# Optimization experiments

Hardware: AMD Instinct MI355X
Metric: run time of the kernel (lower is better)

Reference implementation:

```python
import jax, jax.numpy as jnp
import numpy as np

B, S1, S2, H = 8, 2048, 2048, 1024

def setup_inputs() -> dict:
    key = jax.random.key(0)
    k1, k2, kw, kb = jax.random.split(key, 4)
    hidden1 = jax.random.normal(k1, (B, S1, H), dtype=jnp.float32)
    hidden2 = jax.random.normal(k2, (B, S2, H), dtype=jnp.float32)
    W = jax.random.normal(kw, (H, H), dtype=jnp.float32) * 0.001
    bias = jax.random.normal(kb, (1,), dtype=jnp.float32) * 0.02
    return {"hidden1": hidden1, "hidden2": hidden2, "W": W, "bias": bias}

def reference(hidden1, hidden2, W, bias):
    # weight[b, i, j] = (hidden1 @ W)[b, i, :] . hidden2[b, j, :] + bias
    weight = jnp.einsum('bih,hk,bjk->bij', hidden1, W, hidden2) + bias[0]  # (B, S1, S2)
    # softmax over s1 (dim=1), then transpose-bmm with hidden1 -> (B, S2, H)
    a1 = jax.nn.softmax(weight, axis=1)
    hidden_1 = jnp.einsum('bij,bih->bjh', a1, hidden1)
    # softmax over s2 (dim=2), bmm with hidden2 -> (B, S1, H)
    a2 = jax.nn.softmax(weight, axis=2)
    hidden_2 = jnp.einsum('bij,bjh->bih', a2, hidden2)
    return (hidden_1, hidden_2)
```

## Files before the change

### kernel.cpp

```cpp
#include <hip/hip_runtime.h>
#include <stdint.h>

#define B_  8
#define S1_ 2048
#define S2_ 2048
#define H_  1024

typedef __attribute__((ext_vector_type(8))) short bf16x8;
typedef __attribute__((ext_vector_type(4))) float f32x4;
typedef unsigned short u16;

__device__ __forceinline__ u16 f2bf(float f){
  union { float f; uint32_t v; } x; x.f = f;
  uint32_t r = x.v + 0x7fffu + ((x.v >> 16) & 1u);
  return (u16)(r >> 16);
}
__device__ __forceinline__ u16 f2h(float f){
  union { _Float16 h; u16 u; } c; c.h = (_Float16)f; return c.u;
}
__device__ __forceinline__ float h2f(u16 u){
  union { _Float16 h; u16 u; } c; c.u = u; return (float)c.h;
}
__device__ __forceinline__ uint32_t pk2bf(float lo, float hi){
  uint32_t r;
  asm("v_cvt_pk_bf16_f32 %0, %1, %2" : "=v"(r) : "v"(lo), "v"(hi));
  return r;
}
__device__ __forceinline__ void async16(void* lds, const void* g){
  __builtin_amdgcn_global_load_lds(
      (const __attribute__((address_space(1))) uint32_t*)g,
      (__attribute__((address_space(3))) uint32_t*)lds, 16, 0, 0);
}

__global__ __launch_bounds__(256) void k_cvt_bf16(const float* __restrict__ in,
                                                  u16* __restrict__ out, long n){
  long i = ((long)blockIdx.x * 256 + threadIdx.x) * 8;
  const long stride = (long)gridDim.x * 256 * 8;
  for (; i < n; i += stride){
    float4 a = *(const float4*)(in + i);
    float4 b = *(const float4*)(in + i + 4);
    union { bf16x8 v; uint32_t w[4]; } o;
    o.w[0] = pk2bf(a.x, a.y); o.w[1] = pk2bf(a.z, a.w);
    o.w[2] = pk2bf(b.x, b.y); o.w[3] = pk2bf(b.z, b.w);
    *(bf16x8*)(out + i) = o.v;
  }
}

__global__ __launch_bounds__(256) void k_tcvt(const float* __restrict__ in,
                                              u16* __restrict__ out, int R, int Cc){
  __shared__ u16 t[32][33];
  in  += (long)blockIdx.z * R * Cc;
  out += (long)blockIdx.z * R * Cc;
  const int x = threadIdx.x & 31, y0 = threadIdx.x >> 5;
  const int bx = blockIdx.x * 32, by = blockIdx.y * 32;
  for (int r = y0; r < 32; r += 8) t[r][x] = f2bf(in[(long)(by + r) * Cc + bx + x]);
  __syncthreads();
  for (int r = y0; r < 32; r += 8) out[(long)(bx + r) * R + by + x] = t[x][r];
}

__global__ __launch_bounds__(256) void k_cvtT2(const float* __restrict__ in,
                                               u16* __restrict__ out_n,
                                               u16* __restrict__ out_t, int R, int Cc){
  __shared__ u16 t[64][68];
  in    += (long)blockIdx.z * R * Cc;
  out_n += (long)blockIdx.z * R * Cc;
  out_t += (long)blockIdx.z * R * Cc;
  const int tid = threadIdx.x;
  const int r0 = tid >> 4;
  const int c4 = (tid & 15) * 4;
  const int bx = blockIdx.x * 64;
  const int by = blockIdx.y * 64;
#pragma unroll
  for (int it = 0; it < 4; ++it){
    const int r = it*16 + r0;
    float4 v = *(const float4*)(in + (long)(by + r)*Cc + bx + c4);
    u16 b0 = f2bf(v.x), b1 = f2bf(v.y), b2 = f2bf(v.z), b3 = f2bf(v.w);
    ushort4 o; o.x = b0; o.y = b1; o.z = b2; o.w = b3;
    *(ushort4*)(out_n + (long)(by + r)*Cc + bx + c4) = o;
    t[r][c4] = b0; t[r][c4+1] = b1; t[r][c4+2] = b2; t[r][c4+3] = b3;
  }
  __syncthreads();
#pragma unroll
  for (int it = 0; it < 4; ++it){
    const int c = it*16 + r0;
    ushort4 o;
    o.x = t[c4  ][c]; o.y = t[c4+1][c]; o.z = t[c4+2][c]; o.w = t[c4+3][c];
    *(ushort4*)(out_t + (long)(bx + c)*R + by + c4) = o;
  }
}

template<int OM, bool STATS>
__global__ __launch_bounds__(512) void k_gemm256(
    const u16* __restrict__ A, const u16* __restrict__ Bm, void* __restrict__ Cv,
    int M, int N, int K, long sA, long sB, long sC,
    float* __restrict__ rpmax, float* __restrict__ rpsum,
    float* __restrict__ cpmax, float* __restrict__ cpsum)
{
  const int GX = gridDim.x, GY = gridDim.y;
  const long plane = (long)GX * GY;
  const long tot = plane * gridDim.z;
  const long lin = blockIdx.x + (long)GX * (blockIdx.y + (long)GY * blockIdx.z);
  const long chunk = tot >> 3;
  const long swz = (lin & 7) * chunk + (lin >> 3);
  const int bz = (int)(swz / plane);
  const int rr = (int)(swz % plane);
  const int by_ = rr / GX, bx_ = rr % GX;

  A += (long)bz * sA; Bm += (long)bz * sB;
  __shared__ u16 lds[4 * 16384];
  const int tid = threadIdx.x, lane = tid & 63, w = tid >> 6;
  const int wm = w >> 2, wn = w & 3;
  const int brow = bx_ * 256, bcol = by_ * 256;

  f32x4 acc[8][4];
#pragma unroll
  for (int m=0;m<8;++m)
#pragma unroll
    for (int n=0;n<4;++n) acc[m][n] = (f32x4){0.f,0.f,0.f,0.f};

  const int fr = lane & 15;
  const int g8s = ((lane >> 4) ^ ((lane >> 1) & 3)) * 8;

  const int cc0 = w*128 + lane;
  const int cc1 = w*128 + 64 + lane;
  const int sl0 = (cc0 & 3) ^ ((cc0 >> 3) & 3);
  const int sl1 = (cc1 & 3) ^ ((cc1 >> 3) & 3);
  const u16* gA0 = A  + (long)(brow + (cc0 >> 2)) * K + sl0*8;
  const u16* gA1 = A  + (long)(brow + (cc1 >> 2)) * K + sl1*8;
  const u16* gB0 = Bm + (long)(bcol + (cc0 >> 2)) * K + sl0*8;
  const u16* gB1 = Bm + (long)(bcol + (cc1 >> 2)) * K + sl1*8;
  const int ldA0 = (w*128)*8, ldA1 = (w*128 + 64)*8;

  auto stage = [&](int buf, int t){
    u16* base = lds + buf*16384;
    async16(base + ldA0,        gA0 + t*32);
    async16(base + ldA1,        gA1 + t*32);
    async16(base + 8192 + ldA0, gB0 + t*32);
    async16(base + 8192 + ldA1, gB1 + t*32);
  };
  auto ldfrag = [&](int buf, bf16x8* a, bf16x8* b){
    const u16* At = lds + buf*16384;
    const u16* Bt = At + 8192;
#pragma unroll
    for (int n=0;n<4;++n) b[n] = *(const bf16x8*)(Bt + (wn*64 + n*16 + fr)*32 + g8s);
#pragma unroll
    for (int m=0;m<8;++m) a[m] = *(const bf16x8*)(At + (wm*128 + m*16 + fr)*32 + g8s);
  };

  const int NT = K >> 5;
  stage(0,0); stage(1,1); stage(2,2);
  asm volatile("s_waitcnt vmcnt(4)" ::: "memory");
  __builtin_amdgcn_s_barrier();

  bf16x8 a0[8], b0[4], a1[8], b1[4];
  ldfrag(0, a0, b0);

  for (int t = 0; t < NT; t += 2){
    if (t + 3 < NT) stage((t+3)&3, t+3);
    ldfrag((t+1)&3, a1, b1);
    __builtin_amdgcn_sched_barrier(0);
    __builtin_amdgcn_s_setprio(1);
#pragma unroll
    for (int m=0;m<8;++m)
#pragma unroll
      for (int n=0;n<4;++n)
        acc[m][n] = __builtin_amdgcn_mfma_f32_16x16x32_bf16(a0[m], b0[n], acc[m][n], 0,0,0);
    __builtin_amdgcn_s_setprio(0);
    asm volatile("s_waitcnt vmcnt(4)" ::: "memory");
    __builtin_amdgcn_s_barrier();

    if (t + 4 < NT) stage((t+4)&3, t+4);
    if (t + 2 < NT) ldfrag((t+2)&3, a0, b0);
    __builtin_amdgcn_sched_barrier(0);
    __builtin_amdgcn_s_setprio(1);
#pragma unroll
    for (int m=0;m<8;++m)
#pragma unroll
      for (int n=0;n<4;++n)
        acc[m][n] = __builtin_amdgcn_mfma_f32_16x16x32_bf16(a1[m], b1[n], acc[m][n], 0,0,0);
    __builtin_amdgcn_s_setprio(0);
    if (t + 2 < NT){
      asm volatile("s_waitcnt vmcnt(4)" ::: "memory");
      __builtin_amdgcn_s_barrier();
    }
  }

  const int crow = brow + wm*128 + (lane >> 4) * 4;
  const int ccol = bcol + wn*64 + fr;
  if constexpr (OM == 2){
    float* C = (float*)Cv + (long)bz * sC;
#pragma unroll
    for (int m=0;m<8;++m)
#pragma unroll
      for (int n=0;n<4;++n){
        f32x4 v = acc[m][n];
        float* cp = C + (long)(crow + m*16) * N + ccol + n*16;
#pragma unroll
        for (int q=0;q<4;++q) cp[(long)q*N] = v[q];
      }
  } else {
    u16* C = (u16*)Cv + (long)bz * sC;
#pragma unroll
    for (int m=0;m<8;++m)
#pragma unroll
      for (int n=0;n<4;++n){
        f32x4 v = acc[m][n];
        u16* cp = C + (long)(crow + m*16) * N + ccol + n*16;
#pragma unroll
        for (int q=0;q<4;++q) cp[(long)q*N] = OM ? f2h(v[q]) : f2bf(v[q]);
      }
  }

  if constexpr (STATS){
    const int hi = lane >> 4;
#pragma unroll
    for (int m=0;m<8;++m){
      f32x4 mx = acc[m][0];
#pragma unroll
      for (int n=1;n<4;++n)
#pragma unroll
        for (int q=0;q<4;++q) mx[q] = fmaxf(mx[q], acc[m][n][q]);
#pragma unroll
      for (int off=1; off<16; off<<=1)
#pragma unroll
        for (int q=0;q<4;++q) mx[q] = fmaxf(mx[q], __shfl_xor(mx[q], off));
      f32x4 sm = (f32x4){0.f,0.f,0.f,0.f};
#pragma unroll
      for (int n=0;n<4;++n)
#pragma unroll
        for (int q=0;q<4;++q) sm[q] += __expf(acc[m][n][q] - mx[q]);
#pragma unroll
      for (int off=1; off<16; off<<=1)
#pragma unroll
        for (int q=0;q<4;++q) sm[q] += __shfl_xor(sm[q], off);
      if (fr == 0){
        const int nb = by_*4 + wn;
        const long rb = ((long)bz*32 + nb)*2048 + brow + wm*128 + m*16 + hi*4;
#pragma unroll
        for (int q=0;q<4;++q){ rpmax[rb+q] = mx[q]; rpsum[rb+q] = sm[q]; }
      }
    }
#pragma unroll
    for (int n=0;n<4;++n){
      float mx = acc[0][n][0];
#pragma unroll
      for (int m=0;m<8;++m)
#pragma unroll
        for (int q=0;q<4;++q) mx = fmaxf(mx, acc[m][n][q]);
      mx = fmaxf(mx, __shfl_xor(mx, 16));
      mx = fmaxf(mx, __shfl_xor(mx, 32));
      float sm = 0.f;
#pragma unroll
      for (int m=0;m<8;++m)
#pragma unroll
        for (int q=0;q<4;++q) sm += __expf(acc[m][n][q] - mx);
      sm += __shfl_xor(sm, 16);
      sm += __shfl_xor(sm, 32);
      if (hi == 0){
        const int mb = bx_*2 + wm;
        const long cb = ((long)bz*16 + mb)*2048 + bcol + wn*64 + n*16 + fr;
        cpmax[cb] = mx; cpsum[cb] = sm;
      }
    }
  }
}

__global__ __launch_bounds__(256) void k_combine(
    const float* __restrict__ rpmax, const float* __restrict__ rpsum,
    const float* __restrict__ cpmax, const float* __restrict__ cpsum,
    float* __restrict__ rmax, float* __restrict__ rinv,
    float* __restrict__ cmax, float* __restrict__ cinv)
{
  const long i = (long)blockIdx.x*256 + threadIdx.x;
  const int b = (int)(i >> 11), r = (int)(i & 2047);
  if (blockIdx.y == 0){
    const float* pm = rpmax + ((long)b*32)*2048 + r;
    const float* ps = rpsum + ((long)b*32)*2048 + r;
    float m = -3.4e38f;
#pragma unroll
    for (int k=0;k<32;++k) m = fmaxf(m, pm[(long)k*2048]);
    float s = 0.f;
#pragma unroll
    for (int k=0;k<32;++k) s += ps[(long)k*2048] * __expf(pm[(long)k*2048] - m);
    rmax[i] = m; rinv[i] = 1.f / s;
  } else {
    const float* pm = cpmax + ((long)b*16)*2048 + r;
    const float* ps = cpsum + ((long)b*16)*2048 + r;
    float m = -3.4e38f;
#pragma unroll
    for (int k=0;k<16;++k) m = fmaxf(m, pm[(long)k*2048]);
    float s = 0.f;
#pragma unroll
    for (int k=0;k<16;++k) s += ps[(long)k*2048] * __expf(pm[(long)k*2048] - m);
    cmax[i] = m; cinv[i] = 1.f / s;
  }
}

__global__ __launch_bounds__(256) void k_p1t(u16* __restrict__ Wg, u16* __restrict__ P2,
                                             const float* __restrict__ cmax,
                                             const float* __restrict__ cinv,
                                             const float* __restrict__ rmax,
                                             const float* __restrict__ rinv){
  const int ti = blockIdx.x, tj = blockIdx.y;
  if (tj < ti) return;
  const int b = blockIdx.z;
  u16* S = Wg + (long)b * S1_ * S2_;
  const int jl = threadIdx.x & 63, ig = threadIdx.x >> 6;
  const int I0 = ti*64, J0 = tj*64;
  const float cmA = cmax[b*S2_ + J0 + jl], ciA = cinv[b*S2_ + J0 + jl];
  const float cmB = cmax[b*S2_ + I0 + jl], ciB = cinv[b*S2_ + I0 + jl];
  float ra[16], rc[16];
#pragma unroll
  for (int q=0;q<16;++q) ra[q] = h2f(S[(long)(I0 + ig*16 + q)*S2_ + J0 + jl]);
#pragma unroll
  for (int q=0;q<16;++q) rc[q] = h2f(S[(long)(J0 + ig*16 + q)*S2_ + I0 + jl]);

  if (P2){
    u16* P2b = P2 + (long)b * S1_ * S2_;
#pragma unroll
    for (int q=0;q<16;++q){
      const int r = I0 + ig*16 + q;
      P2b[(long)r*S2_ + J0 + jl] = f2bf(__expf(ra[q] - rmax[b*S1_+r]) * rinv[b*S1_+r]);
    }
    if (ti != tj){
#pragma unroll
      for (int q=0;q<16;++q){
        const int r = J0 + ig*16 + q;
        P2b[(long)r*S2_ + I0 + jl] = f2bf(__expf(rc[q] - rmax[b*S1_+r]) * rinv[b*S1_+r]);
      }
    }
  }

  float a[16], c[16];
#pragma unroll
  for (int q=0;q<16;++q) a[q] = __expf(ra[q] - cmA) * ciA;
#pragma unroll
  for (int q=0;q<16;++q) c[q] = __expf(rc[q] - cmB) * ciB;
  __syncthreads();
  union { bf16x8 v; uint32_t w4[4]; } o0, o1;
#pragma unroll
  for (int k=0;k<4;++k){ o0.w4[k] = pk2bf(a[2*k], a[2*k+1]); o1.w4[k] = pk2bf(a[8+2*k], a[9+2*k]); }
  *(bf16x8*)(S + (long)(J0+jl)*S2_ + I0 + ig*16)     = o0.v;
  *(bf16x8*)(S + (long)(J0+jl)*S2_ + I0 + ig*16 + 8) = o1.v;
#pragma unroll
  for (int k=0;k<4;++k){ o0.w4[k] = pk2bf(c[2*k], c[2*k+1]); o1.w4[k] = pk2bf(c[8+2*k], c[9+2*k]); }
  *(bf16x8*)(S + (long)(I0+jl)*S2_ + J0 + ig*16)     = o0.v;
  *(bf16x8*)(S + (long)(I0+jl)*S2_ + J0 + ig*16 + 8) = o1.v;
}

__global__ __launch_bounds__(256) void k_gemm_h2(
    const u16* __restrict__ Wg, const u16* __restrict__ Bt, float* __restrict__ C,
    const float* __restrict__ rmax, const float* __restrict__ rinv)
{
  const int b = blockIdx.z;
  const u16* A  = Wg + (long)b * S1_ * S2_;
  const u16* Bp = Bt + (long)b * H_ * S2_;
  float* Cp = C + (long)b * S1_ * H_;

  __shared__ u16 As[128*32];
  __shared__ u16 Bs[128*32];
  const int tid = threadIdx.x, lane = tid & 63, w = tid >> 6;
  const int wr = (w >> 1) * 64, wc = (w & 1) * 64;
  const int brow = blockIdx.x * 128, bcol = blockIdx.y * 128;
  f32x4 acc[4][4];
#pragma unroll
  for (int m=0;m<4;++m)
#pragma unroll
    for (int n=0;n<4;++n) acc[m][n] = (f32x4){0.f,0.f,0.f,0.f};

  const int arow = w*16 + (lane >> 2);
  const int scol = (lane & 3) * 8;
  const u16* gA0 = A + (long)(brow + arow) * S2_ + scol;
  const u16* gA1 = gA0 + (long)64 * S2_;
  const float rm0 = rmax[b*S1_ + brow + arow],      ri0 = rinv[b*S1_ + brow + arow];
  const float rm1 = rmax[b*S1_ + brow + arow + 64], ri1 = rinv[b*S1_ + brow + arow + 64];
  u16* wA0 = As + arow*32 + scol;
  u16* wA1 = As + (arow+64)*32 + scol;

  const u16* gb = Bp + (long)(bcol + arow) * S2_ + scol;
  u16* lB0 = Bs + (w*16)*32;  u16* lB1 = Bs + (64 + w*16)*32;

  const int koff = (lane >> 4) * 8;
  const int fr = lane & 15;

  for (int k0 = 0; k0 < S2_; k0 += 32){
    bf16x8 x0 = *(const bf16x8*)(gA0 + k0);
    bf16x8 x1 = *(const bf16x8*)(gA1 + k0);
    async16(lB0, gb);  async16(lB1, gb + (long)64*S2_);
    gb += 32;
    union { bf16x8 v; uint32_t w4[4]; } y0, y1;
#pragma unroll
    for (int k=0;k<4;++k){
      y0.w4[k] = pk2bf(__expf(h2f((u16)x0[2*k])   - rm0) * ri0,
                       __expf(h2f((u16)x0[2*k+1]) - rm0) * ri0);
      y1.w4[k] = pk2bf(__expf(h2f((u16)x1[2*k])   - rm1) * ri1,
                       __expf(h2f((u16)x1[2*k+1]) - rm1) * ri1);
    }
    *(bf16x8*)wA0 = y0.v;
    *(bf16x8*)wA1 = y1.v;
    __syncthreads();
    bf16x8 af[4], bf[4];
#pragma unroll
    for (int m=0;m<4;++m) af[m] = *(const bf16x8*)(As + (wr + m*16 + fr)*32 + koff);
#pragma unroll
    for (int n=0;n<4;++n) bf[n] = *(const bf16x8*)(Bs + (wc + n*16 + fr)*32 + koff);
#pragma unroll
    for (int m=0;m<4;++m)
#pragma unroll
      for (int n=0;n<4;++n)
        acc[m][n] = __builtin_amdgcn_mfma_f32_16x16x32_bf16(af[m], bf[n], acc[m][n], 0,0,0);
    __syncthreads();
  }
  const int crow = brow + wr + (lane >> 4) * 4;
  const int ccol = bcol + wc + fr;
#pragma unroll
  for (int m=0;m<4;++m)
#pragma unroll
    for (int n=0;n<4;++n){
      f32x4 v = acc[m][n];
      float* cp = Cp + (long)(crow + m*16) * H_ + ccol + n*16;
#pragma unroll
      for (int q=0;q<4;++q) cp[(long)q*H_] = v[q];
    }
}

extern "C" void kernel_launch(void* const* d_in, const int* in_sizes, int n_in,
                              void* d_out, int out_size, void* d_ws, size_t ws_size,
                              hipStream_t stream)
{
  const float* h1 = (const float*)d_in[0];
  const float* h2 = (const float*)d_in[1];
  const float* W  = (const float*)d_in[2];
  float* out0 = (float*)d_out;
  float* out1 = out0 + (size_t)B_ * S2_ * H_;

  const long NE = (long)B_ * S1_ * H_;
  const long NS = (long)B_ * S1_ * S2_;

  char* ws = (char*)d_ws;
  size_t off = 0;
  float* rmax = (float*)(ws + off); off += (size_t)B_*S1_*4;
  float* rinv = (float*)(ws + off); off += (size_t)B_*S1_*4;
  float* cmax = (float*)(ws + off); off += (size_t)B_*S2_*4;
  float* cinv = (float*)(ws + off); off += (size_t)B_*S2_*4;
  u16* Wg  = (u16*)(ws + off);
  u16* WTb = Wg;
  off += (size_t)NS*2;
  u16* h1t = (u16*)(ws + off); off += (size_t)NE*2;

  const bool use_p2 = ws_size >= off + (size_t)NS*2;
  u16* P2 = use_p2 ? (u16*)(ws + off) : (u16*)nullptr;
  size_t off2 = off + (use_p2 ? (size_t)NS*2 : 0);
  const bool ws_h2t = ws_size >= off2 + (size_t)NE*2;

  u16* h1b = (u16*)out0;
  u16* h2b = (u16*)out0 + NE;
  u16* h2t = ws_h2t ? (u16*)(ws + off2) : (u16*)out0;
  u16* Qb  = (u16*)out1;
  float* rpmax = (float*)((u16*)out1 + NE);
  float* rpsum = rpmax + (size_t)B_*32*2048;
  float* cpmax = rpsum + (size_t)B_*32*2048;
  float* cpsum = cpmax + (size_t)B_*16*2048;

  k_cvtT2<<<dim3(16,32,8), 256, 0, stream>>>(h1, h1b, h1t, S1_, H_);
  if (ws_h2t){
    k_cvtT2<<<dim3(16,32,8), 256, 0, stream>>>(h2, h2b, h2t, S2_, H_);
  } else {
    k_cvt_bf16<<<dim3(4096), 256, 0, stream>>>(h2, h2b, NE);
  }
  k_tcvt<<<dim3(32,32,1), 256, 0, stream>>>(W, WTb, H_, H_);
  k_gemm256<0,false><<<dim3(8, 4, 8), 512, 0, stream>>>(h1b, WTb, Qb, S1_, H_, H_,
        (long)S1_*H_, 0L, (long)S1_*H_, nullptr, nullptr, nullptr, nullptr);
  if (!ws_h2t){
    k_tcvt<<<dim3(32,64,8), 256, 0, stream>>>(h2, h2t, S2_, H_);
  }
  k_gemm256<1,true><<<dim3(8, 8, 8), 512, 0, stream>>>(Qb, h2b, Wg, S1_, S2_, H_,
        (long)S1_*H_, (long)S2_*H_, (long)S1_*S2_, rpmax, rpsum, cpmax, cpsum);
  k_combine<<<dim3(64, 2), 256, 0, stream>>>(rpmax, rpsum, cpmax, cpsum,
                                             rmax, rinv, cmax, cinv);
  if (use_p2){
    k_p1t<<<dim3(32,32,8), 256, 0, stream>>>(Wg, P2, cmax, cinv, rmax, rinv);
    k_gemm256<2,false><<<dim3(8, 4, 8), 512, 0, stream>>>(P2, h2t, out1, S1_, H_, S2_,
          (long)S1_*S2_, (long)H_*S2_, (long)S1_*H_, nullptr, nullptr, nullptr, nullptr);
  } else {
    k_gemm_h2<<<dim3(16, 8, 8), 256, 0, stream>>>(Wg, h2t, out1, rmax, rinv);
    k_p1t<<<dim3(32,32,8), 256, 0, stream>>>(Wg, (u16*)nullptr, cmax, cinv, rmax, rinv);
  }
  k_gemm256<2,false><<<dim3(8, 4, 8), 512, 0, stream>>>(Wg, h1t, out0, S2_, H_, S1_,
        (long)S1_*S2_, (long)H_*S1_, (long)S2_*H_, nullptr, nullptr, nullptr, nullptr);
}
```

Before: 385.1 us.

## Load B fragments directly from global into registers, staging only A in LDS

The 256x256 GEMM kernel stops staging the B tile in shared memory. Each wave now loads its B MFMA fragments straight from global memory into registers. LDS usage is halved and the B LDS reads disappear. The trade-off is uncoalesced 16-byte global loads and duplicated B reads across the two wm waves, since waves with the same wn share a column. The wait counts and barriers are reworked so the loops run uniformly, with clamped tile indices that issue redundant loads at the tail.

```diff
diff --git a/kernel.cpp b/kernel.cpp
--- a/kernel.cpp
+++ b/kernel.cpp
@@ -107,7 +107,7 @@
   const int by_ = rr / GX, bx_ = rr % GX;
 
   A += (long)bz * sA; Bm += (long)bz * sB;
-  __shared__ u16 lds[4 * 16384];
+  __shared__ u16 lds[4 * 8192];
   const int tid = threadIdx.x, lane = tid & 63, w = tid >> 6;
   const int wm = w >> 2, wn = w & 3;
   const int brow = bx_ * 256, bcol = by_ * 256;
@@ -119,45 +119,49 @@
     for (int n=0;n<4;++n) acc[m][n] = (f32x4){0.f,0.f,0.f,0.f};
 
   const int fr = lane & 15;
-  const int g8s = ((lane >> 4) ^ ((lane >> 1) & 3)) * 8;
+  const int hi = lane >> 4;
+  const int g8s = (hi ^ ((lane >> 1) & 3)) * 8;
 
   const int cc0 = w*128 + lane;
   const int cc1 = w*128 + 64 + lane;
   const int sl0 = (cc0 & 3) ^ ((cc0 >> 3) & 3);
   const int sl1 = (cc1 & 3) ^ ((cc1 >> 3) & 3);
-  const u16* gA0 = A  + (long)(brow + (cc0 >> 2)) * K + sl0*8;
-  const u16* gA1 = A  + (long)(brow + (cc1 >> 2)) * K + sl1*8;
-  const u16* gB0 = Bm + (long)(bcol + (cc0 >> 2)) * K + sl0*8;
-  const u16* gB1 = Bm + (long)(bcol + (cc1 >> 2)) * K + sl1*8;
+  const u16* gA0 = A + (long)(brow + (cc0 >> 2)) * K + sl0*8;
+  const u16* gA1 = A + (long)(brow + (cc1 >> 2)) * K + sl1*8;
   const int ldA0 = (w*128)*8, ldA1 = (w*128 + 64)*8;
 
-  auto stage = [&](int buf, int t){
-    u16* base = lds + buf*16384;
-    async16(base + ldA0,        gA0 + t*32);
-    async16(base + ldA1,        gA1 + t*32);
-    async16(base + 8192 + ldA0, gB0 + t*32);
-    async16(base + 8192 + ldA1, gB1 + t*32);
+  const u16* gBF = Bm + (long)(bcol + wn*64 + fr) * K + hi*8;
+  const long nK16 = (long)16 * K;
+
+  auto stageA = [&](int buf, int t){
+    u16* base = lds + buf*8192;
+    async16(base + ldA0, gA0 + t*32);
+    async16(base + ldA1, gA1 + t*32);
   };
-  auto ldfrag = [&](int buf, bf16x8* a, bf16x8* b){
-    const u16* At = lds + buf*16384;
-    const u16* Bt = At + 8192;
-#pragma unroll
-    for (int n=0;n<4;++n) b[n] = *(const bf16x8*)(Bt + (wn*64 + n*16 + fr)*32 + g8s);
+  auto gloadB = [&](bf16x8* b, int t){
+#pragma unroll
+    for (int n=0;n<4;++n)
+      b[n] = *(const bf16x8*)(gBF + (long)n*nK16 + (long)t*32);
+  };
+  auto ldfragA = [&](int buf, bf16x8* a){
+    const u16* At = lds + buf*8192;
 #pragma unroll
     for (int m=0;m<8;++m) a[m] = *(const bf16x8*)(At + (wm*128 + m*16 + fr)*32 + g8s);
   };
 
   const int NT = K >> 5;
-  stage(0,0); stage(1,1); stage(2,2);
-  asm volatile("s_waitcnt vmcnt(4)" ::: "memory");
+  bf16x8 a0[8], b0[4], a1[8], b1[4];
+  stageA(0,0); stageA(1,1); stageA(2,2);
+  gloadB(b0, 0);
+  asm volatile("s_waitcnt vmcnt(0)" ::: "memory");
   __builtin_amdgcn_s_barrier();
-
-  bf16x8 a0[8], b0[4], a1[8], b1[4];
-  ldfrag(0, a0, b0);
+  ldfragA(0, a0);
 
   for (int t = 0; t < NT; t += 2){
-    if (t + 3 < NT) stage((t+3)&3, t+3);
-    ldfrag((t+1)&3, a1, b1);
+    stageA((t+3)&3, min(t+3, NT-1));
+    gloadB(b1, min(t+1, NT-1));
+    ldfragA((t+1)&3, a1);
+    asm volatile("s_waitcnt vmcnt(6)" ::: "memory");
     __builtin_amdgcn_sched_barrier(0);
     __builtin_amdgcn_s_setprio(1);
 #pragma unroll
@@ -166,11 +170,12 @@
       for (int n=0;n<4;++n)
         acc[m][n] = __builtin_amdgcn_mfma_f32_16x16x32_bf16(a0[m], b0[n], acc[m][n], 0,0,0);
     __builtin_amdgcn_s_setprio(0);
-    asm volatile("s_waitcnt vmcnt(4)" ::: "memory");
     __builtin_amdgcn_s_barrier();
 
-    if (t + 4 < NT) stage((t+4)&3, t+4);
-    if (t + 2 < NT) ldfrag((t+2)&3, a0, b0);
+    stageA((t+4)&3, min(t+4, NT-1));
+    gloadB(b0, min(t+2, NT-1));
+    ldfragA((t+2)&3, a0);
+    asm volatile("s_waitcnt vmcnt(6)" ::: "memory");
     __builtin_amdgcn_sched_barrier(0);
     __builtin_amdgcn_s_setprio(1);
 #pragma unroll
@@ -179,13 +184,10 @@
       for (int n=0;n<4;++n)
         acc[m][n] = __builtin_amdgcn_mfma_f32_16x16x32_bf16(a1[m], b1[n], acc[m][n], 0,0,0);
     __builtin_amdgcn_s_setprio(0);
-    if (t + 2 < NT){
-      asm volatile("s_waitcnt vmcnt(4)" ::: "memory");
-      __builtin_amdgcn_s_barrier();
-    }
-  }
-
-  const int crow = brow + wm*128 + (lane >> 4) * 4;
+    __builtin_amdgcn_s_barrier();
+  }
+
+  const int crow = brow + wm*128 + hi * 4;
   const int ccol = bcol + wn*64 + fr;
   if constexpr (OM == 2){
     float* C = (float*)Cv + (long)bz * sC;
@@ -212,7 +214,6 @@
   }
 
   if constexpr (STATS){
-    const int hi = lane >> 4;
 #pragma unroll
     for (int m=0;m<8;++m){
       f32x4 mx = acc[m][0];
```

New measurement: 501.2 us. 1.3x slower.
